# Optimization experiments

Hardware: AMD Instinct MI355X
Metric: run time of the kernel (lower is better)

Reference implementation:

```python
import jax, jax.numpy as jnp
import numpy as np

NUM_HEADS = 16
ROPE_BASE = 10000.0


def _rope_interleaved(x, cos, sin):
    # x: (B, S, H, hd); cos/sin: (1, S, 1, hd//2)
    x1 = x[..., ::2]
    x2 = x[..., 1::2]
    r1 = x1 * cos - x2 * sin
    r2 = x1 * sin + x2 * cos
    return jnp.stack([r1, r2], axis=-1).reshape(x.shape)


def _rope_tables(seq_len, head_dim, dtype):
    dim = head_dim // 2
    freqs = jnp.exp(-jnp.arange(0, dim, dtype=dtype) * jnp.log(jnp.asarray(ROPE_BASE, dtype)) / dim)
    pos = jnp.arange(seq_len, dtype=dtype)
    angles = pos[:, None] * freqs[None, :]  # (S, hd//2)
    return jnp.cos(angles)[None, :, None, :], jnp.sin(angles)[None, :, None, :]


def setup_inputs() -> dict:
    key = jax.random.key(0)
    ks = jax.random.split(key, 9)
    B, S, D = 2, 2048, 2048
    sc = 1.0 / np.sqrt(D)
    return {
        "x": jax.random.normal(ks[0], (B, S, D), jnp.float32),
        "wq": jax.random.normal(ks[1], (D, D), jnp.float32) * sc,
        "bq": jax.random.normal(ks[2], (D,), jnp.float32) * 0.01,
        "wk": jax.random.normal(ks[3], (D, D), jnp.float32) * sc,
        "bk": jax.random.normal(ks[4], (D,), jnp.float32) * 0.01,
        "wv": jax.random.normal(ks[5], (D, D), jnp.float32) * sc,
        "bv": jax.random.normal(ks[6], (D,), jnp.float32) * 0.01,
        "wo": jax.random.normal(ks[7], (D, D), jnp.float32) * sc,
        "bo": jax.random.normal(ks[8], (D,), jnp.float32) * 0.01,
    }


def reference(x, wq, bq, wk, bk, wv, bv, wo, bo):
    B, S, D = x.shape
    H = NUM_HEADS
    hd = D // H
    # QKV projections (eqx.nn.Linear: y = W @ x + b, weight (out, in))
    q = (x @ wq.T + bq).reshape(B, S, H, hd)
    k = (x @ wk.T + bk).reshape(B, S, H, hd)
    v = (x @ wv.T + bv).reshape(B, S, H, hd)
    # RoPE (interleaved / GPT-NeoX style)
    cos, sin = _rope_tables(S, hd, x.dtype)
    q = _rope_interleaved(q, cos, sin)
    k = _rope_interleaved(k, cos, sin)
    # Causal scaled dot-product attention
    scale = 1.0 / np.sqrt(hd)
    scores = jnp.einsum("bqhd,bkhd->bhqk", q, k) * scale
    causal = jnp.tril(jnp.ones((S, S), dtype=bool))
    scores = jnp.where(causal[None, None, :, :], scores, jnp.finfo(scores.dtype).min)
    attn = jax.nn.softmax(scores, axis=-1)
    out = jnp.einsum("bhqk,bkhd->bqhd", attn, v).reshape(B, S, D)
    return out @ wo.T + bo
```

## Files before the change

kernel.cpp:

```cpp
#include <hip/hip_runtime.h>

typedef unsigned short u16;
typedef short bf16x8 __attribute__((ext_vector_type(8)));
typedef float f32x4 __attribute__((ext_vector_type(4)));

#define B_ 2
#define S_ 2048
#define D_ 2048
#define HD_ 128
#define GW 512
#define KB 32
#define VSTRIDE 40

__device__ __forceinline__ float bf2f(u16 h) {
  unsigned u = ((unsigned)h) << 16;
  return __builtin_bit_cast(float, u);
}
__device__ __forceinline__ u16 f2bf(float f) {
  unsigned u = __builtin_bit_cast(unsigned, f);
  u += 0x7FFF + ((u >> 16) & 1);
  return (u16)(u >> 16);
}
__device__ __forceinline__ bf16x8 cvt8(const float* p) {
  float4 a = *(const float4*)p;
  float4 b = *(const float4*)(p + 4);
  bf16x8 r;
  r[0] = (short)f2bf(a.x); r[1] = (short)f2bf(a.y);
  r[2] = (short)f2bf(a.z); r[3] = (short)f2bf(a.w);
  r[4] = (short)f2bf(b.x); r[5] = (short)f2bf(b.y);
  r[6] = (short)f2bf(b.z); r[7] = (short)f2bf(b.w);
  return r;
}

__device__ __forceinline__ void gload16(const void* g, void* lds) {
  __builtin_amdgcn_global_load_lds(
      (const __attribute__((address_space(1))) unsigned*)g,
      (__attribute__((address_space(3))) unsigned*)lds, 16, 0, 0);
}

__device__ __forceinline__ f32x4 mfma16(bf16x8 a, bf16x8 b, f32x4 c) {
  return __builtin_amdgcn_mfma_f32_16x16x32_bf16(a, b, c, 0, 0, 0);
}

__global__ void k_cvt_all(const float* __restrict__ x, const float* __restrict__ wq,
                          const float* __restrict__ wk, const float* __restrict__ wv,
                          const float* __restrict__ wo, u16* __restrict__ xb,
                          u16* __restrict__ wqkvb, u16* __restrict__ wob) {
  const int slice = blockIdx.y;
  const int i = blockIdx.x * 256 + threadIdx.x;
  const float* src;
  u16* dst;
  int n8;
  if (slice == 0) { src = x; dst = xb; n8 = 1048576; }
  else if (slice == 1) { src = wq; dst = wqkvb; n8 = 524288; }
  else if (slice == 2) { src = wk; dst = wqkvb + 4194304; n8 = 524288; }
  else if (slice == 3) { src = wv; dst = wqkvb + 8388608; n8 = 524288; }
  else { src = wo; dst = wob; n8 = 524288; }
  if (i < n8) *(bf16x8*)(dst + (size_t)i * 8) = cvt8(src + (size_t)i * 8);
}

template <int AM, int WM, int CM>
__device__ __forceinline__ void gemm_body(const void* Ap, const void* Wp,
                                          const float* __restrict__ bias,
                                          void* Cp, int ldc) {
  constexpr int K = 2048;
  __shared__ u16 As[128 * 32];
  __shared__ u16 Bs[128 * 32];
  const int t = threadIdx.x;
  const int w = t >> 6, l = t & 63, lr = l & 15, lg = l >> 4;
  const int m0 = blockIdx.y * 128, n0 = blockIdx.x * 128;
  const int wr = w >> 1, wc = w & 1;

  f32x4 acc[4][4];
#pragma unroll
  for (int i = 0; i < 4; ++i)
#pragma unroll
    for (int j = 0; j < 4; ++j) acc[i][j] = f32x4{0.f, 0.f, 0.f, 0.f};

  const int rowA0 = t >> 2, ko0 = (t & 3) * 8;
  const int rowA1 = (t + 256) >> 2, ko1 = ((t + 256) & 3) * 8;

  for (int kt = 0; kt < K; kt += 32) {
    if constexpr (AM == 1) {
      const u16* A = (const u16*)Ap;
      gload16(A + (size_t)(m0 + rowA0) * K + kt + ko0, (char*)As + (size_t)w * 1024);
      gload16(A + (size_t)(m0 + rowA1) * K + kt + ko1, (char*)As + (size_t)(w + 4) * 1024);
    } else {
      const float* A = (const float*)Ap;
      *(bf16x8*)((char*)As + (size_t)t * 16) = cvt8(A + (size_t)(m0 + rowA0) * K + kt + ko0);
      *(bf16x8*)((char*)As + (size_t)(t + 256) * 16) = cvt8(A + (size_t)(m0 + rowA1) * K + kt + ko1);
    }
    if constexpr (WM == 1) {
      const u16* W = (const u16*)Wp;
      gload16(W + (size_t)(n0 + rowA0) * K + kt + ko0, (char*)Bs + (size_t)w * 1024);
      gload16(W + (size_t)(n0 + rowA1) * K + kt + ko1, (char*)Bs + (size_t)(w + 4) * 1024);
    } else {
      const float* W = (const float*)Wp;
      *(bf16x8*)((char*)Bs + (size_t)t * 16) = cvt8(W + (size_t)(n0 + rowA0) * K + kt + ko0);
      *(bf16x8*)((char*)Bs + (size_t)(t + 256) * 16) = cvt8(W + (size_t)(n0 + rowA1) * K + kt + ko1);
    }
    __syncthreads();

    bf16x8 af[4], bw[4];
#pragma unroll
    for (int i = 0; i < 4; ++i) {
      af[i] = *(const bf16x8*)(As + (size_t)(wr * 64 + i * 16 + lr) * 32 + lg * 8);
      bw[i] = *(const bf16x8*)(Bs + (size_t)(wc * 64 + i * 16 + lr) * 32 + lg * 8);
    }
#pragma unroll
    for (int i = 0; i < 4; ++i)
#pragma unroll
      for (int j = 0; j < 4; ++j)
        acc[i][j] = mfma16(af[i], bw[j], acc[i][j]);
    __syncthreads();
  }

#pragma unroll
  for (int i = 0; i < 4; ++i) {
#pragma unroll
    for (int j = 0; j < 4; ++j) {
      const int col = n0 + wc * 64 + j * 16 + lr;
      const float bv = bias[col];
      const int row = m0 + wr * 64 + i * 16 + lg * 4;
#pragma unroll
      for (int r = 0; r < 4; ++r) {
        if constexpr (CM == 1)
          ((float*)Cp)[(size_t)(row + r) * ldc + col] = acc[i][j][r] + bv;
        else
          ((u16*)Cp)[(size_t)(row + r) * ldc + col] = f2bf(acc[i][j][r] + bv);
      }
    }
  }
}

__global__ __launch_bounds__(256) void k_gemm_qkv_bb(
    const u16* __restrict__ xb, const u16* __restrict__ wqkvb,
    const float* __restrict__ bq, const float* __restrict__ bk,
    const float* __restrict__ bv, u16* __restrict__ q, u16* __restrict__ k,
    u16* __restrict__ v) {
  const int z = blockIdx.z;
  const u16* W = wqkvb + (size_t)z * D_ * D_;
  const float* bias = z == 0 ? bq : (z == 1 ? bk : bv);
  u16* C = z == 0 ? q : (z == 1 ? k : v);
  gemm_body<1, 1, 0>(xb, W, bias, C, D_);
}

__global__ __launch_bounds__(256) void k_gemm_out_bb(
    const u16* __restrict__ ao, const u16* __restrict__ wob,
    const float* __restrict__ bo, float* __restrict__ out) {
  gemm_body<1, 1, 1>(ao, wob, bo, out, D_);
}

__global__ __launch_bounds__(256) void k_gemm_qkv_xb(
    const u16* __restrict__ xb, const float* __restrict__ wq,
    const float* __restrict__ bq, const float* __restrict__ wk,
    const float* __restrict__ bk, const float* __restrict__ wv,
    const float* __restrict__ bv, u16* __restrict__ q, u16* __restrict__ k,
    u16* __restrict__ v) {
  const int z = blockIdx.z;
  const float* W = z == 0 ? wq : (z == 1 ? wk : wv);
  const float* bias = z == 0 ? bq : (z == 1 ? bk : bv);
  u16* C = z == 0 ? q : (z == 1 ? k : v);
  gemm_body<1, 0, 0>(xb, W, bias, C, D_);
}

__global__ __launch_bounds__(256) void k_gemm_out(const u16* __restrict__ ao,
                                                  const float* __restrict__ wo,
                                                  const float* __restrict__ bo,
                                                  float* __restrict__ out) {
  gemm_body<1, 0, 1>(ao, wo, bo, out, D_);
}

__global__ __launch_bounds__(256) void k_gemm_qkv_g(
    const float* __restrict__ x, const float* __restrict__ wq,
    const float* __restrict__ bq, const float* __restrict__ wk,
    const float* __restrict__ bk, const float* __restrict__ wv,
    const float* __restrict__ bv, u16* __restrict__ qg, u16* __restrict__ kg,
    u16* __restrict__ vg, int g) {
  const int z = blockIdx.z;
  const float* W = (z == 0 ? wq : (z == 1 ? wk : wv)) + (size_t)g * GW * D_;
  const float* bias = (z == 0 ? bq : (z == 1 ? bk : bv)) + g * GW;
  u16* C = z == 0 ? qg : (z == 1 ? kg : vg);
  gemm_body<0, 0, 0>(x, W, bias, C, GW);
}

__device__ __forceinline__ void rope_one(u16* p, float cv, float sv) {
  unsigned u = *(const unsigned*)p;
  float x1 = bf2f((u16)(u & 0xffff)), x2 = bf2f((u16)(u >> 16));
  unsigned r = (unsigned)f2bf(x1 * cv - x2 * sv) |
               ((unsigned)f2bf(x1 * sv + x2 * cv) << 16);
  *(unsigned*)p = r;
}

__global__ void k_rope_full(u16* q, u16* kk) {
  const int idx = blockIdx.x * 256 + threadIdx.x;
  const int i = idx & 63;
  const int hh = (idx >> 6) & 15;
  const int bs = idx >> 10;
  const int s = bs & (S_ - 1);
  const float freq = expf(-(float)i * 0.14391157f);
  float sv, cv;
  sincosf((float)s * freq, &sv, &cv);
  const size_t off = (size_t)bs * D_ + (size_t)hh * HD_ + 2 * i;
  rope_one(q + off, cv, sv);
  rope_one(kk + off, cv, sv);
}

__global__ void k_rope_g(u16* q, u16* kk) {
  const int idx = blockIdx.x * 256 + threadIdx.x;
  const int i = idx & 63;
  const int hh = (idx >> 6) & 3;
  const int bs = idx >> 8;
  const int s = bs & (S_ - 1);
  const float freq = expf(-(float)i * 0.14391157f);
  float sv, cv;
  sincosf((float)s * freq, &sv, &cv);
  const size_t off = (size_t)bs * GW + (size_t)hh * HD_ + 2 * i;
  rope_one(q + off, cv, sv);
  rope_one(kk + off, cv, sv);
}

__device__ __forceinline__ void attn_body(const u16* Q, const u16* Kd,
                                          const u16* V, u16* O,
                                          size_t base_in, size_t base_out,
                                          int ld_in, int ld_out, int q0) {
  const int t = threadIdx.x, w = t >> 6, l = t & 63, lr = l & 15, lg = l >> 4;

  __shared__ u16 Ks[KB * HD_];
  __shared__ u16 Vt[HD_ * VSTRIDE];
  __shared__ u16 Ps[4][16 * KB];

  bf16x8 qf[4];
  {
    const u16* qp = Q + base_in + (size_t)(q0 + w * 16 + lr) * ld_in;
#pragma unroll
    for (int ds = 0; ds < 4; ++ds)
      qf[ds] = *(const bf16x8*)(qp + ds * 32 + lg * 8);
  }

  f32x4 oacc[8];
#pragma unroll
  for (int f = 0; f < 8; ++f) oacc[f] = f32x4{0.f, 0.f, 0.f, 0.f};
  float mrow[4] = {-1e30f, -1e30f, -1e30f, -1e30f};
  float lrow[4] = {0.f, 0.f, 0.f, 0.f};

  const int q_hi = q0 + w * 16 + 15;
  const int ntiles = (q0 + 64) / KB;
  const float sc = 0.08838834764831845f;

  for (int tkv = 0; tkv < ntiles; ++tkv) {
    const int kv0 = tkv * KB;
#pragma unroll
    for (int r = 0; r < 2; ++r) {
      const int c = t + 256 * r;
      const int row = c >> 4, c16 = c & 15;
      const int gc = c16 ^ (row & 7);
      gload16(Kd + base_in + (size_t)(kv0 + row) * ld_in + gc * 8,
              (char*)Ks + (size_t)(w + 4 * r) * 1024);
    }
#pragma unroll
    for (int r = 0; r < 2; ++r) {
      const int c = t + 256 * r;
      const int kk = c & 31, d0 = (c >> 5) * 8;
      bf16x8 vv = *(const bf16x8*)(V + base_in + (size_t)(kv0 + kk) * ld_in + d0);
#pragma unroll
      for (int j = 0; j < 8; ++j) Vt[(size_t)(d0 + j) * VSTRIDE + kk] = (u16)vv[j];
    }
    __syncthreads();

    if (kv0 <= q_hi) {
      f32x4 s0 = {0.f, 0.f, 0.f, 0.f}, s1 = {0.f, 0.f, 0.f, 0.f};
#pragma unroll
      for (int ds = 0; ds < 4; ++ds) {
        const int ch = (ds * 4 + lg) ^ (lr & 7);
        bf16x8 k0 = *(const bf16x8*)(Ks + (size_t)lr * HD_ + ch * 8);
        bf16x8 k1 = *(const bf16x8*)(Ks + (size_t)(16 + lr) * HD_ + ch * 8);
        s0 = mfma16(qf[ds], k0, s0);
        s1 = mfma16(qf[ds], k1, s1);
      }
      float p0[4], p1[4], pmax[4];
#pragma unroll
      for (int j = 0; j < 4; ++j) {
        const int qrow = q0 + w * 16 + lg * 4 + j;
        float a0 = s0[j] * sc;
        if (kv0 + lr > qrow) a0 = -1e30f;
        float a1 = s1[j] * sc;
        if (kv0 + 16 + lr > qrow) a1 = -1e30f;
        p0[j] = a0;
        p1[j] = a1;
        pmax[j] = fmaxf(a0, a1);
      }
#pragma unroll
      for (int mk = 1; mk <= 8; mk <<= 1)
#pragma unroll
        for (int j = 0; j < 4; ++j)
          pmax[j] = fmaxf(pmax[j], __shfl_xor(pmax[j], mk, 64));
      float scl[4], rsum[4];
#pragma unroll
      for (int j = 0; j < 4; ++j) {
        const float mn = fmaxf(mrow[j], pmax[j]);
        scl[j] = __expf(mrow[j] - mn);
        mrow[j] = mn;
        const float e0 = __expf(p0[j] - mn);
        const float e1 = __expf(p1[j] - mn);
        p0[j] = e0;
        p1[j] = e1;
        rsum[j] = e0 + e1;
      }
#pragma unroll
      for (int mk = 1; mk <= 8; mk <<= 1)
#pragma unroll
        for (int j = 0; j < 4; ++j) rsum[j] += __shfl_xor(rsum[j], mk, 64);
#pragma unroll
      for (int j = 0; j < 4; ++j) lrow[j] = lrow[j] * scl[j] + rsum[j];
#pragma unroll
      for (int f = 0; f < 8; ++f)
#pragma unroll
        for (int j = 0; j < 4; ++j) oacc[f][j] *= scl[j];
#pragma unroll
      for (int j = 0; j < 4; ++j) {
        const int prow = lg * 4 + j;
        Ps[w][prow * KB + lr] = f2bf(p0[j]);
        Ps[w][prow * KB + 16 + lr] = f2bf(p1[j]);
      }
      bf16x8 pf = *(const bf16x8*)(&Ps[w][lr * KB + lg * 8]);
#pragma unroll
      for (int f = 0; f < 8; ++f) {
        bf16x8 vf = *(const bf16x8*)(Vt + (size_t)(f * 16 + lr) * VSTRIDE + lg * 8);
        oacc[f] = mfma16(pf, vf, oacc[f]);
      }
    }
    __syncthreads();
  }

  float inv[4];
#pragma unroll
  for (int j = 0; j < 4; ++j) inv[j] = 1.0f / lrow[j];
  u16* Op = O + base_out;
#pragma unroll
  for (int f = 0; f < 8; ++f)
#pragma unroll
    for (int j = 0; j < 4; ++j)
      Op[(size_t)(q0 + w * 16 + lg * 4 + j) * ld_out + f * 16 + lr] =
          f2bf(oacc[f][j] * inv[j]);
}

__global__ __launch_bounds__(256) void k_attn_full(const u16* Q, const u16* Kd,
                                                   const u16* V, u16* O) {
  const int lin = blockIdx.y * gridDim.x + blockIdx.x;
  const int work = (lin & 7) * 64 + (lin >> 3);
  const int bh = work >> 4;
  const int pr = work & 15;
  const int b = bh >> 4, h = bh & 15;
  const size_t base = ((size_t)b * S_) * D_ + (size_t)h * HD_;
  attn_body(Q, Kd, V, O, base, base, D_, D_, 64 * (31 - pr));
  attn_body(Q, Kd, V, O, base, base, D_, D_, 64 * pr);
}

__global__ __launch_bounds__(256) void k_attn_g(const u16* __restrict__ Q,
                                                const u16* __restrict__ Kd,
                                                const u16* __restrict__ V,
                                                u16* __restrict__ O, int g) {
  const int by = blockIdx.y;
  const int b = by >> 2, hh = by & 3;
  const size_t base_in = ((size_t)b * S_) * GW + (size_t)hh * HD_;
  const size_t base_out = ((size_t)b * S_) * D_ + (size_t)(g * 4 + hh) * HD_;
  attn_body(Q, Kd, V, O, base_in, base_out, GW, D_, blockIdx.x * 64);
}

extern "C" void kernel_launch(void* const* d_in, const int* in_sizes, int n_in,
                              void* d_out, int out_size, void* d_ws,
                              size_t ws_size, hipStream_t stream) {
  (void)in_sizes; (void)n_in; (void)out_size;
  const float* x = (const float*)d_in[0];
  const float* wq = (const float*)d_in[1];
  const float* bq = (const float*)d_in[2];
  const float* wk = (const float*)d_in[3];
  const float* bk = (const float*)d_in[4];
  const float* wv = (const float*)d_in[5];
  const float* bv = (const float*)d_in[6];
  const float* wo = (const float*)d_in[7];
  const float* bo = (const float*)d_in[8];
  float* out = (float*)d_out;

  const size_t XB = (size_t)B_ * S_ * D_ * 2;
  const size_t WB3 = 3 * (size_t)D_ * D_ * 2;
  const size_t WB1 = (size_t)D_ * D_ * 2;
  char* ws = (char*)d_ws;
  char* ob = (char*)d_out;

  u16 *xb, *q, *k, *v, *wqkvb = nullptr, *wob = nullptr;
  int tier;
  if (ws_size >= 4 * XB + WB3 + WB1) {
    xb = (u16*)ws; q = (u16*)(ws + XB); k = (u16*)(ws + 2 * XB);
    v = (u16*)(ws + 3 * XB);
    wqkvb = (u16*)(ws + 4 * XB); wob = (u16*)(ws + 4 * XB + WB3);
    tier = 1;
  } else if (ws_size >= 3 * XB + WB3 + WB1) {
    xb = (u16*)ob;
    q = (u16*)ws; k = (u16*)(ws + XB); v = (u16*)(ws + 2 * XB);
    wqkvb = (u16*)(ws + 3 * XB); wob = (u16*)(ws + 3 * XB + WB3);
    tier = 1;
  } else if (ws_size >= 2 * XB + WB3 + WB1) {
    xb = (u16*)ob; v = (u16*)(ob + XB);
    q = (u16*)ws; k = (u16*)(ws + XB);
    wqkvb = (u16*)(ws + 2 * XB); wob = (u16*)(ws + 2 * XB + WB3);
    tier = 1;
  } else if (ws_size >= 2 * XB) {
    xb = (u16*)ob; v = (u16*)(ob + XB);
    q = (u16*)ws; k = (u16*)(ws + XB);
    tier = 2;
  } else {
    tier = 3;
  }

  if (tier == 1) {
    dim3 gc(4096, 5);
    k_cvt_all<<<gc, 256, 0, stream>>>(x, wq, wk, wv, wo, xb, wqkvb, wob);
    dim3 g1(16, 32, 3);
    k_gemm_qkv_bb<<<g1, 256, 0, stream>>>(xb, wqkvb, bq, bk, bv, q, k, v);
    k_rope_full<<<16384, 256, 0, stream>>>(q, k);
    dim3 g2(16, 32);
    k_attn_full<<<g2, 256, 0, stream>>>(q, k, v, q);
    dim3 g3(16, 32);
    k_gemm_out_bb<<<g3, 256, 0, stream>>>(q, wob, bo, out);
  } else if (tier == 2) {
    dim3 gc(4096, 1);
    k_cvt_all<<<gc, 256, 0, stream>>>(x, wq, wk, wv, wo, xb, xb, xb);
    dim3 g1(16, 32, 3);
    k_gemm_qkv_xb<<<g1, 256, 0, stream>>>(xb, wq, bq, wk, bk, wv, bv, q, k, v);
    k_rope_full<<<16384, 256, 0, stream>>>(q, k);
    dim3 g2(16, 32);
    k_attn_full<<<g2, 256, 0, stream>>>(q, k, v, q);
    dim3 g3(16, 32);
    k_gemm_out<<<g3, 256, 0, stream>>>(q, wo, bo, out);
  } else {
    u16* qg = (u16*)ob;
    u16* kg = qg + (size_t)(B_ * S_) * GW;
    u16* vg = kg + (size_t)(B_ * S_) * GW;
    u16* ao = (u16*)ws;
    for (int g = 0; g < 4; ++g) {
      dim3 g1(4, 32, 3);
      k_gemm_qkv_g<<<g1, 256, 0, stream>>>(x, wq, bq, wk, bk, wv, bv, qg, kg, vg, g);
      k_rope_g<<<4096, 256, 0, stream>>>(qg, kg);
      dim3 g2(32, 8);
      k_attn_g<<<g2, 256, 0, stream>>>(qg, kg, vg, ao, g);
    }
    dim3 g3(16, 32);
    k_gemm_out<<<g3, 256, 0, stream>>>(ao, wo, bo, out);
  }
}
```

Baseline: 340.3 us.

## Widen attention KV tile to 64 and compute transposed scores for per-lane softmax

Doubles the KV tile from 32 to 64 keys. S is now computed as K·Q^T so each lane owns one query row, and the row max and sum need only two cross-lane shuffles. The causal mask is applied only on diagonal tiles, and V is transposed into shared memory with packed 32-bit stores. The aim is fewer barriers and tile iterations and cheaper softmax reductions. The cost is more shared memory, more registers per thread and extra shuffles to broadcast scale factors.

```diff
diff --git a/kernel.cpp b/kernel.cpp
--- a/kernel.cpp
+++ b/kernel.cpp
@@ -9,8 +9,9 @@
 #define D_ 2048
 #define HD_ 128
 #define GW 512
-#define KB 32
-#define VSTRIDE 40
+#define KB 64
+#define VST 72
+#define PST 72
 
 __device__ __forceinline__ float bf2f(u16 h) {
   unsigned u = ((unsigned)h) << 16;
@@ -227,8 +228,8 @@
   const int t = threadIdx.x, w = t >> 6, l = t & 63, lr = l & 15, lg = l >> 4;
 
   __shared__ u16 Ks[KB * HD_];
-  __shared__ u16 Vt[HD_ * VSTRIDE];
-  __shared__ u16 Ps[4][16 * KB];
+  __shared__ u16 Vt[HD_ * VST];
+  __shared__ u16 Ps[4][16 * PST];
 
   bf16x8 qf[4];
   {
@@ -241,17 +242,16 @@
   f32x4 oacc[8];
 #pragma unroll
   for (int f = 0; f < 8; ++f) oacc[f] = f32x4{0.f, 0.f, 0.f, 0.f};
-  float mrow[4] = {-1e30f, -1e30f, -1e30f, -1e30f};
-  float lrow[4] = {0.f, 0.f, 0.f, 0.f};
-
-  const int q_hi = q0 + w * 16 + 15;
-  const int ntiles = (q0 + 64) / KB;
+  float mrow = -1e30f, lrow = 0.f;
+
+  const int qrow = q0 + w * 16 + lr;
+  const int ntiles = q0 / KB + 1;
   const float sc = 0.08838834764831845f;
 
   for (int tkv = 0; tkv < ntiles; ++tkv) {
     const int kv0 = tkv * KB;
 #pragma unroll
-    for (int r = 0; r < 2; ++r) {
+    for (int r = 0; r < 4; ++r) {
       const int c = t + 256 * r;
       const int row = c >> 4, c16 = c & 15;
       const int gc = c16 ^ (row & 7);
@@ -261,88 +261,90 @@
 #pragma unroll
     for (int r = 0; r < 2; ++r) {
       const int c = t + 256 * r;
-      const int kk = c & 31, d0 = (c >> 5) * 8;
-      bf16x8 vv = *(const bf16x8*)(V + base_in + (size_t)(kv0 + kk) * ld_in + d0);
-#pragma unroll
-      for (int j = 0; j < 8; ++j) Vt[(size_t)(d0 + j) * VSTRIDE + kk] = (u16)vv[j];
+      const int kk2 = (c & 31) * 2, d0 = (c >> 5) * 8;
+      bf16x8 v0 = *(const bf16x8*)(V + base_in + (size_t)(kv0 + kk2) * ld_in + d0);
+      bf16x8 v1 = *(const bf16x8*)(V + base_in + (size_t)(kv0 + kk2 + 1) * ld_in + d0);
+#pragma unroll
+      for (int j = 0; j < 8; ++j) {
+        unsigned pk = (unsigned)(unsigned short)v0[j] |
+                      ((unsigned)(unsigned short)v1[j] << 16);
+        *(unsigned*)&Vt[(size_t)(d0 + j) * VST + kk2] = pk;
+      }
     }
     __syncthreads();
 
-    if (kv0 <= q_hi) {
-      f32x4 s0 = {0.f, 0.f, 0.f, 0.f}, s1 = {0.f, 0.f, 0.f, 0.f};
+    float p[16];
+#pragma unroll
+    for (int h = 0; h < 4; ++h) {
+      f32x4 s = {0.f, 0.f, 0.f, 0.f};
 #pragma unroll
       for (int ds = 0; ds < 4; ++ds) {
         const int ch = (ds * 4 + lg) ^ (lr & 7);
-        bf16x8 k0 = *(const bf16x8*)(Ks + (size_t)lr * HD_ + ch * 8);
-        bf16x8 k1 = *(const bf16x8*)(Ks + (size_t)(16 + lr) * HD_ + ch * 8);
-        s0 = mfma16(qf[ds], k0, s0);
-        s1 = mfma16(qf[ds], k1, s1);
+        bf16x8 kf = *(const bf16x8*)(Ks + (size_t)(h * 16 + lr) * HD_ + ch * 8);
+        s = mfma16(kf, qf[ds], s);
       }
-      float p0[4], p1[4], pmax[4];
-#pragma unroll
-      for (int j = 0; j < 4; ++j) {
-        const int qrow = q0 + w * 16 + lg * 4 + j;
-        float a0 = s0[j] * sc;
-        if (kv0 + lr > qrow) a0 = -1e30f;
-        float a1 = s1[j] * sc;
-        if (kv0 + 16 + lr > qrow) a1 = -1e30f;
-        p0[j] = a0;
-        p1[j] = a1;
-        pmax[j] = fmaxf(a0, a1);
-      }
-#pragma unroll
-      for (int mk = 1; mk <= 8; mk <<= 1)
-#pragma unroll
-        for (int j = 0; j < 4; ++j)
-          pmax[j] = fmaxf(pmax[j], __shfl_xor(pmax[j], mk, 64));
-      float scl[4], rsum[4];
-#pragma unroll
-      for (int j = 0; j < 4; ++j) {
-        const float mn = fmaxf(mrow[j], pmax[j]);
-        scl[j] = __expf(mrow[j] - mn);
-        mrow[j] = mn;
-        const float e0 = __expf(p0[j] - mn);
-        const float e1 = __expf(p1[j] - mn);
-        p0[j] = e0;
-        p1[j] = e1;
-        rsum[j] = e0 + e1;
-      }
-#pragma unroll
-      for (int mk = 1; mk <= 8; mk <<= 1)
-#pragma unroll
-        for (int j = 0; j < 4; ++j) rsum[j] += __shfl_xor(rsum[j], mk, 64);
-#pragma unroll
-      for (int j = 0; j < 4; ++j) lrow[j] = lrow[j] * scl[j] + rsum[j];
-#pragma unroll
-      for (int f = 0; f < 8; ++f)
-#pragma unroll
-        for (int j = 0; j < 4; ++j) oacc[f][j] *= scl[j];
-#pragma unroll
-      for (int j = 0; j < 4; ++j) {
-        const int prow = lg * 4 + j;
-        Ps[w][prow * KB + lr] = f2bf(p0[j]);
-        Ps[w][prow * KB + 16 + lr] = f2bf(p1[j]);
-      }
-      bf16x8 pf = *(const bf16x8*)(&Ps[w][lr * KB + lg * 8]);
-#pragma unroll
-      for (int f = 0; f < 8; ++f) {
-        bf16x8 vf = *(const bf16x8*)(Vt + (size_t)(f * 16 + lr) * VSTRIDE + lg * 8);
-        oacc[f] = mfma16(pf, vf, oacc[f]);
-      }
+#pragma unroll
+      for (int r = 0; r < 4; ++r) p[h * 4 + r] = s[r] * sc;
+    }
+    if (kv0 + KB - 1 > q0 + w * 16) {
+#pragma unroll
+      for (int h = 0; h < 4; ++h)
+#pragma unroll
+        for (int r = 0; r < 4; ++r)
+          if (kv0 + h * 16 + lg * 4 + r > qrow) p[h * 4 + r] = -1e30f;
+    }
+    float pm = p[0];
+#pragma unroll
+    for (int i = 1; i < 16; ++i) pm = fmaxf(pm, p[i]);
+    pm = fmaxf(pm, __shfl_xor(pm, 16, 64));
+    pm = fmaxf(pm, __shfl_xor(pm, 32, 64));
+    const float mn = fmaxf(mrow, pm);
+    const float scl = __expf(mrow - mn);
+    mrow = mn;
+    float rs = 0.f;
+#pragma unroll
+    for (int i = 0; i < 16; ++i) {
+      p[i] = __expf(p[i] - mn);
+      rs += p[i];
+    }
+    rs += __shfl_xor(rs, 16, 64);
+    rs += __shfl_xor(rs, 32, 64);
+    lrow = lrow * scl + rs;
+    float sj[4];
+#pragma unroll
+    for (int j = 0; j < 4; ++j) sj[j] = __shfl(scl, lg * 4 + j, 64);
+#pragma unroll
+    for (int f = 0; f < 8; ++f)
+#pragma unroll
+      for (int j = 0; j < 4; ++j) oacc[f][j] *= sj[j];
+#pragma unroll
+    for (int h = 0; h < 4; ++h)
+#pragma unroll
+      for (int r = 0; r < 4; ++r)
+        Ps[w][lr * PST + h * 16 + lg * 4 + r] = f2bf(p[h * 4 + r]);
+    bf16x8 pf0 = *(const bf16x8*)&Ps[w][lr * PST + lg * 8];
+    bf16x8 pf1 = *(const bf16x8*)&Ps[w][lr * PST + 32 + lg * 8];
+#pragma unroll
+    for (int f = 0; f < 8; ++f) {
+      bf16x8 vf0 = *(const bf16x8*)&Vt[(size_t)(f * 16 + lr) * VST + lg * 8];
+      bf16x8 vf1 = *(const bf16x8*)&Vt[(size_t)(f * 16 + lr) * VST + 32 + lg * 8];
+      oacc[f] = mfma16(pf0, vf0, oacc[f]);
+      oacc[f] = mfma16(pf1, vf1, oacc[f]);
     }
     __syncthreads();
   }
 
-  float inv[4];
-#pragma unroll
-  for (int j = 0; j < 4; ++j) inv[j] = 1.0f / lrow[j];
+  const float inv = 1.0f / lrow;
+  float ij[4];
+#pragma unroll
+  for (int j = 0; j < 4; ++j) ij[j] = __shfl(inv, lg * 4 + j, 64);
   u16* Op = O + base_out;
 #pragma unroll
   for (int f = 0; f < 8; ++f)
 #pragma unroll
     for (int j = 0; j < 4; ++j)
       Op[(size_t)(q0 + w * 16 + lg * 4 + j) * ld_out + f * 16 + lr] =
-          f2bf(oacc[f][j] * inv[j]);
+          f2bf(oacc[f][j] * ij[j]);
 }
 
 __global__ __launch_bounds__(256) void k_attn_full(const u16* Q, const u16* Kd,
```

New measurement: 293.0 us. 1.16x faster.
